# Kernel optimization log

Hardware: AMD Instinct MI355X
Metric: run time of the kernel (lower is better)

Reference implementation:

```python
import jax, jax.numpy as jnp
import numpy as np

B, N, H, W, C = 512, 16, 84, 84, 3
CNN_OUT, ATTN, GH, HEADS, POS, A_DIM = 256, 64, 128, 2, 3, 3
IN_GAT = CNN_OUT + POS  # 259
FLAT = 64 * 16 * 16     # conv output flat dim for 84x84 input


def setup_inputs() -> dict:
    key = jax.random.key(0)
    ks = jax.random.split(key, 16)
    s = 0.05
    return dict(
        cam=jax.random.uniform(ks[0], (B, H, W, C), jnp.float32),
        pos=jax.random.normal(ks[1], (B, POS), jnp.float32),
        team_pos=jax.random.normal(ks[2], (B, N, POS), jnp.float32) * 10.0,
        agent_idx=jax.random.randint(ks[3], (B,), 0, N),
        W1=jax.random.normal(ks[4], (32, C, 8, 8), jnp.float32) * s, b1=jnp.zeros((32,), jnp.float32),
        W2=jax.random.normal(ks[5], (64, 32, 4, 4), jnp.float32) * s, b2=jnp.zeros((64,), jnp.float32),
        W3=jax.random.normal(ks[6], (64, 64, 3, 3), jnp.float32) * s, b3=jnp.zeros((64,), jnp.float32),
        Wp=jax.random.normal(ks[7], (FLAT, CNN_OUT), jnp.float32) * 0.01, bp=jnp.zeros((CNN_OUT,), jnp.float32),
        Wid=jax.random.normal(ks[8], (1, ATTN), jnp.float32) * s, bid=jnp.zeros((ATTN,), jnp.float32),
        Wg=jax.random.normal(ks[9], (IN_GAT, HEADS * GH), jnp.float32) * s,
        a_src=jax.random.normal(ks[10], (HEADS, GH), jnp.float32) * s,
        a_dst=jax.random.normal(ks[11], (HEADS, GH), jnp.float32) * s,
        Wh1=jax.random.normal(ks[12], (HEADS * GH + ATTN, 256), jnp.float32) * s, bh1=jnp.zeros((256,), jnp.float32),
        Wh2=jax.random.normal(ks[13], (256, 2 * A_DIM), jnp.float32) * s, bh2=jnp.zeros((2 * A_DIM,), jnp.float32),
    )


def _conv(x, w, b, stride):
    y = jax.lax.conv_general_dilated(x, w, (stride, stride), 'VALID',
                                     dimension_numbers=('NCHW', 'OIHW', 'NCHW'))
    return jax.nn.relu(y + b[None, :, None, None])


def reference(cam, pos, team_pos, agent_idx, W1, b1, W2, b2, W3, b3, Wp, bp,
              Wid, bid, Wg, a_src, a_dst, Wh1, bh1, Wh2, bh2):
    # CNN encoder (NHWC -> NCHW)
    x = jnp.transpose(cam, (0, 3, 1, 2))
    x = _conv(x, W1, b1, 2)   # [B,32,39,39]
    x = _conv(x, W2, b2, 2)   # [B,64,18,18]
    x = _conv(x, W3, b3, 1)   # [B,64,16,16]
    cam_feat = jax.nn.relu(x.reshape(x.shape[0], -1) @ Wp + bp)  # [B,256]

    # per-node features: broadcast ego cam feat + relative team positions
    rel_pos = team_pos - pos[:, None, :]                                     # [B,N,3]
    node_feats = jnp.concatenate(
        [jnp.broadcast_to(cam_feat[:, None, :], (B, N, CNN_OUT)), rel_pos], axis=-1)  # [B,N,259]

    # adjacency: within 100m, no self-loops, self-loop added for isolated nodes
    dist = jnp.linalg.norm(team_pos[:, :, None, :] - team_pos[:, None, :, :], axis=-1)  # [B,N,N]
    eye = jnp.eye(N, dtype=node_feats.dtype)
    adj = (dist < 100.0).astype(node_feats.dtype) * (1.0 - eye)
    need_self = (adj.sum(axis=2) == 0).astype(adj.dtype)                     # [B,N]
    adj = adj + eye[None] * need_self[..., None]

    # dense multi-head GAT layer
    hN = (node_feats @ Wg).reshape(B, N, HEADS, GH)                          # [B,N,H,D]
    src = jnp.einsum('bnhd,hd->bnh', hN, a_src)
    dst = jnp.einsum('bnhd,hd->bnh', hN, a_dst)
    e = jax.nn.leaky_relu(src[:, :, None, :] + dst[:, None, :, :], 0.2)      # [B,i,j,H]
    e = jnp.where(adj[..., None] > 0, e, -1e9)
    alpha = jax.nn.softmax(e, axis=2)
    h = jnp.einsum('bijh,bjhd->bihd', alpha, hN).reshape(B, N, HEADS * GH)   # [B,N,256]
    h = jax.nn.elu(h)
    h = jnp.nan_to_num(h, nan=0.0, posinf=0.0, neginf=0.0)

    # agent-id embedding, fuse, gather own node, policy head
    id_emb = jax.nn.relu(agent_idx.astype(jnp.float32)[:, None] @ Wid + bid)  # [B,64]
    fused = jnp.concatenate([h, jnp.broadcast_to(id_emb[:, None, :], (B, N, ATTN))], axis=-1)  # [B,N,320]
    agent_feat = fused[jnp.arange(B), agent_idx]                             # [B,320]
    z = jax.nn.relu(agent_feat @ Wh1 + bh1)
    logits = z @ Wh2 + bh2                                                    # [B,6]
    return logits
```

## Files before the change

kernel.cpp:

```cpp
#include <hip/hip_runtime.h>


typedef __attribute__((ext_vector_type(8))) short bf16x8;
typedef __attribute__((ext_vector_type(4))) float f32x4;

union U4 { uint4 v; unsigned int u[4]; bf16x8 h; };

__device__ __forceinline__ unsigned short f2bf(float x) {
    unsigned int u = __float_as_uint(x);
    return (unsigned short)((u + 0x7FFFu + ((u >> 16) & 1u)) >> 16);
}
__device__ __forceinline__ unsigned int pack2(float lo, float hi) {
    return (unsigned int)f2bf(lo) | ((unsigned int)f2bf(hi) << 16);
}
__device__ __forceinline__ bf16x8 loadA(const unsigned int* __restrict__ W, int k8, int M, int oc) {
    U4 r; r.v = *(const uint4*)(W + (((size_t)k8 * M + oc) << 2));
    return r.h;
}
__device__ __forceinline__ bf16x8 loadB4(const unsigned int* __restrict__ base, size_t idx) {
    U4 r; r.v = *(const uint4*)(base + (idx << 2));
    return r.h;
}
#define MFMA(a, b, c) __builtin_amdgcn_mfma_f32_16x16x32_bf16((a), (b), (c), 0, 0, 0)

__device__ __forceinline__ int xcd_swz(int L, int nwg) {
    int q = nwg >> 3, r = nwg & 7;
    int x = L & 7, i = L >> 3;
    return (x < r ? x * (q + 1) : r * (q + 1) + (x - r) * q) + i;
}

__device__ __forceinline__ void storeK(unsigned int* __restrict__ out,
                                       size_t row, size_t BC, size_t bcol,
                                       int lg, unsigned int u0, unsigned int u1) {
    uint2 v; v.x = u0; v.y = u1;
    *(uint2*)(out + ((row * BC + bcol) << 2) + ((lg & 1) << 1)) = v;
}

__global__ __launch_bounds__(256) void prepack(
    const float* __restrict__ W1, const float* __restrict__ W2,
    const float* __restrict__ W3, const float* __restrict__ Wp,
    const float* __restrict__ Wg, const float* __restrict__ Wh1,
    unsigned int* __restrict__ W1t, unsigned int* __restrict__ W2t,
    unsigned int* __restrict__ W3t, unsigned int* __restrict__ Wpt,
    unsigned int* __restrict__ Wgt, unsigned int* __restrict__ Wh1t)
{
    int i = blockIdx.x * 256 + threadIdx.x;
    if (i < 4096) {
        int j2 = i & 3, oc = (i >> 2) & 31, k8 = i >> 7;
        int kh = k8 >> 2, kwp = k8 & 3;
        float w[2];
        #pragma unroll
        for (int e = 0; e < 2; e++) {
            int jj = 2 * j2 + e;
            int kwlo = jj >> 2, c = jj & 3;
            w[e] = (c == 3) ? 0.f
                 : W1[((oc * 3 + c) * 8 + kh) * 8 + 2 * kwp + kwlo];
        }
        W1t[i] = pack2(w[0], w[1]);
    } else if (i < 20480) {
        int j = i - 4096;
        int j2 = j & 3, oc = (j >> 2) & 63, k8 = j >> 8;
        int tap = k8 >> 2, ic = (k8 & 3) * 8 + 2 * j2;
        int kh = tap >> 2, kw = tap & 3;
        float a = W2[((oc * 32 + ic) * 4 + kh) * 4 + kw];
        float b = W2[((oc * 32 + ic + 1) * 4 + kh) * 4 + kw];
        W2t[j] = pack2(a, b);
    } else if (i < 38912) {
        int j = i - 20480;
        int j2 = j & 3, oc = (j >> 2) & 63, k8 = j >> 8;
        int tap = k8 >> 3, ic = (k8 & 7) * 8 + 2 * j2;
        int kh = tap / 3, kw = tap % 3;
        float a = W3[((oc * 64 + ic) * 3 + kh) * 3 + kw];
        float b = W3[((oc * 64 + ic + 1) * 3 + kh) * 3 + kw];
        W3t[j] = pack2(a, b);
    } else if (i < 2136064) {
        int j = i - 38912;
        int j2 = j & 3, n = (j >> 2) & 255, k8 = j >> 10;
        int s3 = k8 >> 3, oc = (k8 & 7) * 8 + 2 * j2;
        float a = Wp[(size_t)(oc * 256 + s3) * 256 + n];
        float b = Wp[(size_t)((oc + 1) * 256 + s3) * 256 + n];
        Wpt[j] = pack2(a, b);
    } else if (i < 2168832) {
        int j = i - 2136064;
        int j2 = j & 3, m = (j >> 2) & 255, k8 = j >> 10;
        int k = k8 * 8 + 2 * j2;
        Wgt[j] = pack2(Wg[k * 256 + m], Wg[(k + 1) * 256 + m]);
    } else if (i < 2209792) {
        int j = i - 2168832;
        int j2 = j & 3, m = (j >> 2) & 255, k8 = j >> 10;
        int k = k8 * 8 + 2 * j2;
        Wh1t[j] = pack2(Wh1[k * 256 + m], Wh1[(k + 1) * 256 + m]);
    }
}

__global__ __launch_bounds__(256) void transpose_cam(
    const float* __restrict__ cam, unsigned int* __restrict__ camq, int b0, int BC)
{
    __shared__ float lds[32][253];
    int yy = blockIdx.x;
    int bb = blockIdx.y * 32;
    int t = threadIdx.x;
    for (int f = t; f < 8064; f += 256) {
        int b = f / 252, p = f - b * 252;
        lds[b][p] = cam[(size_t)(b0 + bb + b) * 21168 + yy * 252 + p];
    }
    __syncthreads();
    for (int g = t; g < 1344; g += 256) {
        int b = g & 31, xp = g >> 5;
        const float* l = &lds[b][6 * xp];
        uint4 u;
        u.x = pack2(l[0], l[1]);
        u.y = pack2(l[2], 0.f);
        u.z = pack2(l[3], l[4]);
        u.w = pack2(l[5], 0.f);
        *(uint4*)(camq + (((size_t)(yy * 42 + xp) * BC + bb + b) << 2)) = u;
    }
}

__global__ __launch_bounds__(256, 3) void conv1_pair(
    const unsigned int* __restrict__ in32, const unsigned int* __restrict__ Wt,
    const float* __restrict__ bias, unsigned int* __restrict__ out32,
    int BC, int nspat)
{
    int wgid = xcd_swz(blockIdx.x, gridDim.x);
    int s = wgid % nspat;
    int bq = wgid / nspat;
    int ohp = s / 39, ow = s - ohp * 39;
    int oh0 = 2 * ohp;
    const bool has2 = (oh0 + 1) < 39;
    int wv = threadIdx.x >> 6, l = threadIdx.x & 63;
    int lg = l >> 4, lc = l & 15;
    const size_t sBC = (size_t)BC;
    size_t base = (size_t)bq * 256 + wv * 64 + lc;
    f32x4 acc0[2][4] = {}, acc1[2][4] = {};
    bf16x8 Ar0[2], Ar1[2];
    #pragma unroll
    for (int t = 0; t < 10; t++) {
        const int par = t & 1;
        bf16x8 B[4];
        if (t < 8 || has2) {
            size_t row = (size_t)((2 * oh0 + t) * 42 + ow + lg);
            #pragma unroll
            for (int g = 0; g < 4; g++)
                B[g] = loadB4(in32, row * sBC + base + g * 16);
        }
        if (t >= 2 && has2) {
            #pragma unroll
            for (int g = 0; g < 4; g++) {
                acc1[0][g] = MFMA(Ar0[par], B[g], acc1[0][g]);
                acc1[1][g] = MFMA(Ar1[par], B[g], acc1[1][g]);
            }
        }
        if (t < 8) {
            bf16x8 An0 = loadA(Wt, t * 4 + lg, 32, lc);
            bf16x8 An1 = loadA(Wt, t * 4 + lg, 32, 16 + lc);
            #pragma unroll
            for (int g = 0; g < 4; g++) {
                acc0[0][g] = MFMA(An0, B[g], acc0[0][g]);
                acc0[1][g] = MFMA(An1, B[g], acc0[1][g]);
            }
            Ar0[par] = An0; Ar1[par] = An1;
        }
    }
    int s0 = oh0 * 39 + ow;
    #pragma unroll
    for (int m = 0; m < 2; m++) {
        float4 bv = *(const float4*)(bias + m * 16 + lg * 4);
        size_t row = (size_t)s0 * 4 + 2 * m + (lg >> 1);
        #pragma unroll
        for (int g = 0; g < 4; g++) {
            f32x4 a = acc0[m][g];
            unsigned int u0 = pack2(fmaxf(a.x + bv.x, 0.f), fmaxf(a.y + bv.y, 0.f));
            unsigned int u1 = pack2(fmaxf(a.z + bv.z, 0.f), fmaxf(a.w + bv.w, 0.f));
            storeK(out32, row, sBC, base + g * 16, lg, u0, u1);
        }
        if (has2) {
            size_t row1 = row + 4 * 39;
            #pragma unroll
            for (int g = 0; g < 4; g++) {
                f32x4 a = acc1[m][g];
                unsigned int u0 = pack2(fmaxf(a.x + bv.x, 0.f), fmaxf(a.y + bv.y, 0.f));
                unsigned int u1 = pack2(fmaxf(a.z + bv.z, 0.f), fmaxf(a.w + bv.w, 0.f));
                storeK(out32, row1, sBC, base + g * 16, lg, u0, u1);
            }
        }
    }
}

__global__ __launch_bounds__(256, 3) void conv2_mfma(
    const unsigned int* __restrict__ in32, const unsigned int* __restrict__ Wt,
    const float* __restrict__ bias, unsigned int* __restrict__ out32,
    int BC, int nspat)
{
    int wgid = xcd_swz(blockIdx.x, gridDim.x);
    int s = wgid % nspat;
    int bq = wgid / nspat;
    int oh = s / 18, ow = s - oh * 18;
    int wv = threadIdx.x >> 6, l = threadIdx.x & 63;
    int lg = l >> 4, lc = l & 15;
    const size_t sBC = (size_t)BC;
    size_t base = (size_t)bq * 256 + wv * 64 + lc;
    f32x4 acc[4][4] = {};
    int ybase = 2 * oh, xbase = 2 * ow;
    #pragma unroll 1
    for (int sp = 0; sp < 8; sp++) {
        const int s0 = 2 * sp, s1 = s0 + 1;
        bf16x8 A0[4], A1[4], B0[4], B1[4];
        #pragma unroll
        for (int m = 0; m < 4; m++) {
            A0[m] = loadA(Wt, s0 * 4 + lg, 64, m * 16 + lc);
            A1[m] = loadA(Wt, s1 * 4 + lg, 64, m * 16 + lc);
        }
        {
            const int kh = s0 >> 2, kw = s0 & 3;
            size_t row = (size_t)(((ybase + kh) * 39 + xbase + kw) * 4 + lg);
            #pragma unroll
            for (int g = 0; g < 4; g++)
                B0[g] = loadB4(in32, row * sBC + base + g * 16);
        }
        {
            const int kh = s1 >> 2, kw = s1 & 3;
            size_t row = (size_t)(((ybase + kh) * 39 + xbase + kw) * 4 + lg);
            #pragma unroll
            for (int g = 0; g < 4; g++)
                B1[g] = loadB4(in32, row * sBC + base + g * 16);
        }
        #pragma unroll
        for (int m = 0; m < 4; m++)
            #pragma unroll
            for (int g = 0; g < 4; g++)
                acc[m][g] = MFMA(A0[m], B0[g], acc[m][g]);
        #pragma unroll
        for (int m = 0; m < 4; m++)
            #pragma unroll
            for (int g = 0; g < 4; g++)
                acc[m][g] = MFMA(A1[m], B1[g], acc[m][g]);
    }
    #pragma unroll
    for (int m = 0; m < 4; m++) {
        float4 bv = *(const float4*)(bias + m * 16 + lg * 4);
        size_t row = (size_t)s * 8 + 2 * m + (lg >> 1);
        #pragma unroll
        for (int g = 0; g < 4; g++) {
            f32x4 a = acc[m][g];
            unsigned int u0 = pack2(fmaxf(a.x + bv.x, 0.f), fmaxf(a.y + bv.y, 0.f));
            unsigned int u1 = pack2(fmaxf(a.z + bv.z, 0.f), fmaxf(a.w + bv.w, 0.f));
            storeK(out32, row, sBC, base + g * 16, lg, u0, u1);
        }
    }
}

__global__ __launch_bounds__(256, 3) void conv3_mfma(
    const unsigned int* __restrict__ in32, const unsigned int* __restrict__ Wt,
    const float* __restrict__ bias, unsigned int* __restrict__ out32,
    int BC, int nspat)
{
    int wgid = xcd_swz(blockIdx.x, gridDim.x);
    int s = wgid % nspat;
    int bq = wgid / nspat;
    int oh = s >> 4, ow = s & 15;
    int wv = threadIdx.x >> 6, l = threadIdx.x & 63;
    int lg = l >> 4, lc = l & 15;
    const size_t sBC = (size_t)BC;
    size_t base = (size_t)bq * 256 + wv * 64 + lc;
    f32x4 acc[4][4] = {};
    #pragma unroll 1
    for (int sp = 0; sp < 9; sp++) {
        const int s0 = 2 * sp, s1 = s0 + 1;
        const int kh = sp / 3, kw = sp - kh * 3;
        bf16x8 A0[4], A1[4], B0[4], B1[4];
        #pragma unroll
        for (int m = 0; m < 4; m++) {
            A0[m] = loadA(Wt, s0 * 4 + lg, 64, m * 16 + lc);
            A1[m] = loadA(Wt, s1 * 4 + lg, 64, m * 16 + lc);
        }
        size_t row0 = (size_t)(((oh + kh) * 18 + ow + kw) * 8 + lg);
        #pragma unroll
        for (int g = 0; g < 4; g++) {
            B0[g] = loadB4(in32, row0 * sBC + base + g * 16);
            B1[g] = loadB4(in32, (row0 + 4) * sBC + base + g * 16);
        }
        #pragma unroll
        for (int m = 0; m < 4; m++)
            #pragma unroll
            for (int g = 0; g < 4; g++)
                acc[m][g] = MFMA(A0[m], B0[g], acc[m][g]);
        #pragma unroll
        for (int m = 0; m < 4; m++)
            #pragma unroll
            for (int g = 0; g < 4; g++)
                acc[m][g] = MFMA(A1[m], B1[g], acc[m][g]);
    }
    #pragma unroll
    for (int m = 0; m < 4; m++) {
        float4 bv = *(const float4*)(bias + m * 16 + lg * 4);
        size_t row = (size_t)s * 8 + 2 * m + (lg >> 1);
        #pragma unroll
        for (int g = 0; g < 4; g++) {
            f32x4 a = acc[m][g];
            unsigned int u0 = pack2(fmaxf(a.x + bv.x, 0.f), fmaxf(a.y + bv.y, 0.f));
            unsigned int u1 = pack2(fmaxf(a.z + bv.z, 0.f), fmaxf(a.w + bv.w, 0.f));
            storeK(out32, row, sBC, base + g * 16, lg, u0, u1);
        }
    }
}

__global__ __launch_bounds__(256, 3) void proj_mfma(
    const unsigned int* __restrict__ x3, const unsigned int* __restrict__ Wpt,
    float* __restrict__ partial, int BC)
{
    int wgid = xcd_swz(blockIdx.x, gridDim.x);
    int rem = wgid & 127;
    int b128 = wgid >> 7;
    int mq = rem & 3;
    int kseg = rem >> 2;
    int wv = threadIdx.x >> 6, l = threadIdx.x & 63;
    int lg = l >> 4, lc = l & 15;
    const size_t sBC = (size_t)BC;
    size_t base = (size_t)b128 * 128 + wv * 32 + lc;
    f32x4 acc[4][2] = {};
    #pragma unroll 1
    for (int sp = 0; sp < 8; sp++) {
        const int k8b = kseg * 64 + sp * 8;
        bf16x8 A0[4], A1[4], B0[2], B1[2];
        #pragma unroll
        for (int m = 0; m < 4; m++) {
            A0[m] = loadA(Wpt, k8b + lg, 256, mq * 64 + m * 16 + lc);
            A1[m] = loadA(Wpt, k8b + 4 + lg, 256, mq * 64 + m * 16 + lc);
        }
        #pragma unroll
        for (int g = 0; g < 2; g++) {
            B0[g] = loadB4(x3, (size_t)(k8b + lg) * sBC + base + g * 16);
            B1[g] = loadB4(x3, (size_t)(k8b + 4 + lg) * sBC + base + g * 16);
        }
        #pragma unroll
        for (int m = 0; m < 4; m++)
            #pragma unroll
            for (int g = 0; g < 2; g++)
                acc[m][g] = MFMA(A0[m], B0[g], acc[m][g]);
        #pragma unroll
        for (int m = 0; m < 4; m++)
            #pragma unroll
            for (int g = 0; g < 2; g++)
                acc[m][g] = MFMA(A1[m], B1[g], acc[m][g]);
    }
    #pragma unroll
    for (int m = 0; m < 4; m++) {
        size_t row4 = (size_t)kseg * 64 + mq * 16 + m * 4 + lg;
        #pragma unroll
        for (int g = 0; g < 2; g++)
            *(f32x4*)(partial + ((row4 * sBC + base + g * 16) << 2)) = acc[m][g];
    }
}

__global__ __launch_bounds__(256) void reduce_k(
    const float* __restrict__ partial, const float* __restrict__ bp,
    unsigned int* __restrict__ cf16, int b0, int BC, int bcShift)
{
    int i = blockIdx.x * 256 + threadIdx.x;
    int bl = i & (BC - 1);
    int k8 = i >> bcShift;
    f32x4 S0 = {}, S1 = {};
    for (int seg = 0; seg < 32; seg++) {
        const float* p = partial + (((size_t)(seg * 64 + k8 * 2) * BC + bl) << 2);
        S0 += *(const f32x4*)p;
        S1 += *(const f32x4*)(p + (BC << 2));
    }
    int n = k8 * 8;
    uint4 u;
    u.x = pack2(fmaxf(S0.x + bp[n + 0], 0.f), fmaxf(S0.y + bp[n + 1], 0.f));
    u.y = pack2(fmaxf(S0.z + bp[n + 2], 0.f), fmaxf(S0.w + bp[n + 3], 0.f));
    u.z = pack2(fmaxf(S1.x + bp[n + 4], 0.f), fmaxf(S1.y + bp[n + 5], 0.f));
    u.w = pack2(fmaxf(S1.z + bp[n + 6], 0.f), fmaxf(S1.w + bp[n + 7], 0.f));
    *(uint4*)(cf16 + (((size_t)k8 * 512 + b0 + bl) << 2)) = u;
}

__global__ __launch_bounds__(64) void gat_prep(
    const unsigned int* __restrict__ cf16, const unsigned int* __restrict__ Wgt,
    float* __restrict__ hNb)
{
    int mq = blockIdx.x, bq = blockIdx.y;
    int l = threadIdx.x, lg = l >> 4, lc = l & 15;
    size_t bcol = (size_t)bq * 32 + lc;
    f32x4 acc[4][2] = {};
    #pragma unroll
    for (int sp = 0; sp < 4; sp++) {
        const int s0 = 2 * sp, s1 = s0 + 1;
        bf16x8 A0[4], A1[4], B0[2], B1[2];
        #pragma unroll
        for (int m = 0; m < 4; m++) {
            A0[m] = loadA(Wgt, s0 * 4 + lg, 256, mq * 64 + m * 16 + lc);
            A1[m] = loadA(Wgt, s1 * 4 + lg, 256, mq * 64 + m * 16 + lc);
        }
        #pragma unroll
        for (int g = 0; g < 2; g++) {
            B0[g] = loadB4(cf16, (size_t)(s0 * 4 + lg) * 512 + bcol + g * 16);
            B1[g] = loadB4(cf16, (size_t)(s1 * 4 + lg) * 512 + bcol + g * 16);
        }
        #pragma unroll
        for (int m = 0; m < 4; m++) {
            acc[m][0] = MFMA(A0[m], B0[0], acc[m][0]);
            acc[m][1] = MFMA(A0[m], B0[1], acc[m][1]);
            acc[m][0] = MFMA(A1[m], B1[0], acc[m][0]);
            acc[m][1] = MFMA(A1[m], B1[1], acc[m][1]);
        }
    }
    #pragma unroll
    for (int m = 0; m < 4; m++) {
        #pragma unroll
        for (int g = 0; g < 2; g++) {
            size_t b = (size_t)bq * 32 + g * 16 + lc;
            int row0 = mq * 64 + m * 16 + lg * 4;
            *(f32x4*)(hNb + b * 256 + row0) = acc[m][g];
        }
    }
}

__global__ __launch_bounds__(256) void gat_mid(
    const float* __restrict__ hNb, const float* __restrict__ pos,
    const float* __restrict__ tpos, const int* __restrict__ aidx,
    const float* __restrict__ Wg, const float* __restrict__ asrc, const float* __restrict__ adst,
    const float* __restrict__ Wid, const float* __restrict__ bid,
    unsigned int* __restrict__ af16)
{
    int b = blockIdx.x, t = threadIdx.x;
    __shared__ float hN[16][256];
    __shared__ float srcv[16][2], dstv[16][2];
    __shared__ float alpha[16][2];
    __shared__ float af[320];
    __shared__ unsigned int adjm_s;

    int ai = aidx[b];
    float basev = hNb[(size_t)b * 256 + t];
    float rw0 = Wg[65536 + t], rw1 = Wg[65792 + t], rw2 = Wg[66048 + t];
    float px = pos[b * 3 + 0], py = pos[b * 3 + 1], pz = pos[b * 3 + 2];
    for (int n = 0; n < 16; n++) {
        float r0 = tpos[(b * 16 + n) * 3 + 0] - px;
        float r1 = tpos[(b * 16 + n) * 3 + 1] - py;
        float r2 = tpos[(b * 16 + n) * 3 + 2] - pz;
        hN[n][t] = basev + r0 * rw0 + r1 * rw1 + r2 * rw2;
    }

    if (t < 64) {
        bool on = false;
        if (t < 16 && t != ai) {
            float dx = tpos[(b * 16 + ai) * 3 + 0] - tpos[(b * 16 + t) * 3 + 0];
            float dy = tpos[(b * 16 + ai) * 3 + 1] - tpos[(b * 16 + t) * 3 + 1];
            float dz = tpos[(b * 16 + ai) * 3 + 2] - tpos[(b * 16 + t) * 3 + 2];
            on = (dx * dx + dy * dy + dz * dz) < 10000.0f;
        }
        unsigned long long m = __ballot(on);
        if (t == 0) adjm_s = (m == 0ull) ? (1u << ai) : (unsigned int)m;
    }
    __syncthreads();

    {
        int p = t >> 3, sub = t & 7;
        int j = p >> 1, h = p & 1;
        float s1 = 0.f, s2 = 0.f;
        #pragma unroll
        for (int dd = 0; dd < 16; dd++) {
            int d = h * 128 + sub * 16 + dd;
            float v = hN[j][d];
            s1 += v * asrc[d];
            s2 += v * adst[d];
        }
        s1 += __shfl_xor(s1, 1); s1 += __shfl_xor(s1, 2); s1 += __shfl_xor(s1, 4);
        s2 += __shfl_xor(s2, 1); s2 += __shfl_xor(s2, 2); s2 += __shfl_xor(s2, 4);
        if (sub == 0) { srcv[j][h] = s1; dstv[j][h] = s2; }
    }
    __syncthreads();

    if (t < 32) {
        int j = t & 15, h = t >> 4;
        unsigned int am = adjm_s;
        float e = srcv[ai][h] + dstv[j][h];
        e = (e > 0.f) ? e : 0.2f * e;
        e = ((am >> j) & 1u) ? e : -1e9f;
        float mx = e;
        mx = fmaxf(mx, __shfl_xor(mx, 1));
        mx = fmaxf(mx, __shfl_xor(mx, 2));
        mx = fmaxf(mx, __shfl_xor(mx, 4));
        mx = fmaxf(mx, __shfl_xor(mx, 8));
        float ex = __expf(e - mx);
        float sm = ex;
        sm += __shfl_xor(sm, 1); sm += __shfl_xor(sm, 2);
        sm += __shfl_xor(sm, 4); sm += __shfl_xor(sm, 8);
        alpha[j][h] = ex / sm;
    }
    __syncthreads();

    {
        int h = t >> 7;
        float o = 0.f;
        #pragma unroll
        for (int j = 0; j < 16; j++) o += alpha[j][h] * hN[j][t];
        o = (o > 0.f) ? o : (__expf(o) - 1.f);
        af[t] = o;
    }
    if (t < 64) {
        float v = (float)ai * Wid[t] + bid[t];
        af[256 + t] = fmaxf(v, 0.f);
    }
    __syncthreads();

    if (t < 40) {
        uint4 u;
        u.x = pack2(af[t * 8 + 0], af[t * 8 + 1]);
        u.y = pack2(af[t * 8 + 2], af[t * 8 + 3]);
        u.z = pack2(af[t * 8 + 4], af[t * 8 + 5]);
        u.w = pack2(af[t * 8 + 6], af[t * 8 + 7]);
        *(uint4*)(af16 + (((size_t)t * 512 + b) << 2)) = u;
    }
}

__global__ __launch_bounds__(64) void head_mfma(
    const unsigned int* __restrict__ af16, const unsigned int* __restrict__ Wh1t,
    const float* __restrict__ bh1, float* __restrict__ zf)
{
    int mq = blockIdx.x, bq = blockIdx.y;
    int l = threadIdx.x, lg = l >> 4, lc = l & 15;
    size_t bcol = (size_t)bq * 32 + lc;
    f32x4 acc[4][2] = {};
    #pragma unroll
    for (int sp = 0; sp < 5; sp++) {
        const int s0 = 2 * sp, s1 = s0 + 1;
        bf16x8 A0[4], A1[4], B0[2], B1[2];
        #pragma unroll
        for (int m = 0; m < 4; m++) {
            A0[m] = loadA(Wh1t, s0 * 4 + lg, 256, mq * 64 + m * 16 + lc);
            A1[m] = loadA(Wh1t, s1 * 4 + lg, 256, mq * 64 + m * 16 + lc);
        }
        #pragma unroll
        for (int g = 0; g < 2; g++) {
            B0[g] = loadB4(af16, (size_t)(s0 * 4 + lg) * 512 + bcol + g * 16);
            B1[g] = loadB4(af16, (size_t)(s1 * 4 + lg) * 512 + bcol + g * 16);
        }
        #pragma unroll
        for (int m = 0; m < 4; m++) {
            acc[m][0] = MFMA(A0[m], B0[0], acc[m][0]);
            acc[m][1] = MFMA(A0[m], B0[1], acc[m][1]);
            acc[m][0] = MFMA(A1[m], B1[0], acc[m][0]);
            acc[m][1] = MFMA(A1[m], B1[1], acc[m][1]);
        }
    }
    #pragma unroll
    for (int m = 0; m < 4; m++) {
        int row0 = mq * 64 + m * 16 + lg * 4;
        float4 bv = *(const float4*)(bh1 + row0);
        #pragma unroll
        for (int g = 0; g < 2; g++) {
            f32x4 a = acc[m][g];
            size_t b = (size_t)bq * 32 + g * 16 + lc;
            float* pp = zf + (size_t)row0 * 512 + b;
            pp[0]       = fmaxf(a.x + bv.x, 0.f);
            pp[512]     = fmaxf(a.y + bv.y, 0.f);
            pp[2 * 512] = fmaxf(a.z + bv.z, 0.f);
            pp[3 * 512] = fmaxf(a.w + bv.w, 0.f);
        }
    }
}

__global__ __launch_bounds__(256) void logits_k(
    const float* __restrict__ zf, const float* __restrict__ Wh2,
    const float* __restrict__ bh2, float* __restrict__ out)
{
    __shared__ float Ws[1536];
    int t = threadIdx.x;
    int b = blockIdx.x * 256 + t;
    for (int f = t; f < 1536; f += 256) Ws[f] = Wh2[f];
    __syncthreads();
    float acc[6];
    #pragma unroll
    for (int j = 0; j < 6; j++) acc[j] = bh2[j];
    for (int k = 0; k < 256; k++) {
        float zv = zf[(size_t)k * 512 + b];
        #pragma unroll
        for (int j = 0; j < 6; j++) acc[j] += zv * Ws[k * 6 + j];
    }
    #pragma unroll
    for (int j = 0; j < 6; j++) out[b * 6 + j] = acc[j];
}

extern "C" void kernel_launch(void* const* d_in, const int* in_sizes, int n_in,
                              void* d_out, int out_size, void* d_ws, size_t ws_size,
                              hipStream_t stream)
{
    const float* cam  = (const float*)d_in[0];
    const float* pos  = (const float*)d_in[1];
    const float* tpos = (const float*)d_in[2];
    const int*   aidx = (const int*)d_in[3];
    const float* W1   = (const float*)d_in[4];
    const float* b1   = (const float*)d_in[5];
    const float* W2   = (const float*)d_in[6];
    const float* b2   = (const float*)d_in[7];
    const float* W3   = (const float*)d_in[8];
    const float* b3   = (const float*)d_in[9];
    const float* Wp   = (const float*)d_in[10];
    const float* bp   = (const float*)d_in[11];
    const float* Wid  = (const float*)d_in[12];
    const float* bid  = (const float*)d_in[13];
    const float* Wg   = (const float*)d_in[14];
    const float* asrc = (const float*)d_in[15];
    const float* adst = (const float*)d_in[16];
    const float* Wh1  = (const float*)d_in[17];
    const float* bh1  = (const float*)d_in[18];
    const float* Wh2  = (const float*)d_in[19];
    const float* bh2  = (const float*)d_in[20];
    float* out = (float*)d_out;

    int BC = 256;
    if (((size_t)54832 * 512 + 2619392) * 4 <= ws_size) BC = 512;
    int bcShift = (BC == 512) ? 9 : 8;
    int nbq2 = BC >> 8;

    unsigned int* ws32 = (unsigned int*)d_ws;
    unsigned int* RA  = ws32;
    unsigned int* RB  = RA + (size_t)14112 * BC;
    unsigned int* RC  = RB + (size_t)24336 * BC;
    float*        RD  = (float*)(RC + (size_t)8192 * BC);
    unsigned int* W1t = (unsigned int*)(RD + (size_t)8192 * BC);
    unsigned int* W2t  = W1t + 4096;
    unsigned int* W3t  = W2t + 16384;
    unsigned int* Wpt  = W3t + 18432;
    unsigned int* Wgt  = Wpt + 2097152;
    unsigned int* Wh1t = Wgt + 32768;
    unsigned int* cf16 = Wh1t + 40960;
    float*        hNb  = (float*)(cf16 + 65536);
    unsigned int* af16 = (unsigned int*)(hNb + 131072);
    float*        zf   = (float*)(af16 + 81920);

    prepack<<<8632, 256, 0, stream>>>(W1, W2, W3, Wp, Wg, Wh1,
                                      W1t, W2t, W3t, Wpt, Wgt, Wh1t);

    for (int b0 = 0; b0 < 512; b0 += BC) {
        transpose_cam<<<dim3(84, BC / 32), 256, 0, stream>>>(cam, RA, b0, BC);
        conv1_pair<<<780 * nbq2, 256, 0, stream>>>(RA, W1t, b1, RB, BC, 780);
        conv2_mfma<<<324 * nbq2, 256, 0, stream>>>(RB, W2t, b2, RA, BC, 324);
        conv3_mfma<<<256 * nbq2, 256, 0, stream>>>(RA, W3t, b3, RC, BC, 256);
        proj_mfma<<<128 * (BC >> 7), 256, 0, stream>>>(RC, Wpt, RD, BC);
        reduce_k<<<(32 * BC) / 256, 256, 0, stream>>>(RD, bp, cf16, b0, BC, bcShift);
    }
    gat_prep<<<dim3(4, 16), 64, 0, stream>>>(cf16, Wgt, hNb);
    gat_mid<<<512, 256, 0, stream>>>(hNb, pos, tpos, aidx, Wg, asrc, adst,
                                     Wid, bid, af16);
    head_mfma<<<dim3(4, 16), 64, 0, stream>>>(af16, Wh1t, bh1, zf);
    logits_k<<<2, 256, 0, stream>>>(zf, Wh2, bh2, out);
}
```

Measured before the change: 148.3 us.

## Halve conv/proj workgroup size, shrink split-K, and fuse head with logits

conv2 and conv3 now run 128-thread workgroups covering 128 batch columns each, which doubles the grid. The projection GEMM also uses 128-thread workgroups over 64 columns, but each one handles twice the K range, so there are 16 K segments instead of 32. This halves the partial-sum buffer and the reduction work. The head MFMA and logits kernels are fused into one kernel that keeps z in shared memory, removing a launch and a global round trip. The trade-off is more workgroups and less weight reuse per group in the convs, plus fewer parallel K segments in proj.

```diff
diff --git a/kernel.cpp b/kernel.cpp
--- a/kernel.cpp
+++ b/kernel.cpp
@@ -187,7 +187,7 @@
     }
 }
 
-__global__ __launch_bounds__(256, 3) void conv2_mfma(
+__global__ __launch_bounds__(128, 3) void conv2_mfma(
     const unsigned int* __restrict__ in32, const unsigned int* __restrict__ Wt,
     const float* __restrict__ bias, unsigned int* __restrict__ out32,
     int BC, int nspat)
@@ -199,7 +199,7 @@
     int wv = threadIdx.x >> 6, l = threadIdx.x & 63;
     int lg = l >> 4, lc = l & 15;
     const size_t sBC = (size_t)BC;
-    size_t base = (size_t)bq * 256 + wv * 64 + lc;
+    size_t base = (size_t)bq * 128 + wv * 64 + lc;
     f32x4 acc[4][4] = {};
     int ybase = 2 * oh, xbase = 2 * ow;
     #pragma unroll 1
@@ -250,7 +250,7 @@
     }
 }
 
-__global__ __launch_bounds__(256, 3) void conv3_mfma(
+__global__ __launch_bounds__(128, 3) void conv3_mfma(
     const unsigned int* __restrict__ in32, const unsigned int* __restrict__ Wt,
     const float* __restrict__ bias, unsigned int* __restrict__ out32,
     int BC, int nspat)
@@ -262,7 +262,7 @@
     int wv = threadIdx.x >> 6, l = threadIdx.x & 63;
     int lg = l >> 4, lc = l & 15;
     const size_t sBC = (size_t)BC;
-    size_t base = (size_t)bq * 256 + wv * 64 + lc;
+    size_t base = (size_t)bq * 128 + wv * 64 + lc;
     f32x4 acc[4][4] = {};
     #pragma unroll 1
     for (int sp = 0; sp < 9; sp++) {
@@ -305,23 +305,23 @@
     }
 }
 
-__global__ __launch_bounds__(256, 3) void proj_mfma(
+__global__ __launch_bounds__(128, 3) void proj_mfma(
     const unsigned int* __restrict__ x3, const unsigned int* __restrict__ Wpt,
     float* __restrict__ partial, int BC)
 {
     int wgid = xcd_swz(blockIdx.x, gridDim.x);
-    int rem = wgid & 127;
-    int b128 = wgid >> 7;
+    int rem = wgid & 63;
+    int b64 = wgid >> 6;
     int mq = rem & 3;
     int kseg = rem >> 2;
     int wv = threadIdx.x >> 6, l = threadIdx.x & 63;
     int lg = l >> 4, lc = l & 15;
     const size_t sBC = (size_t)BC;
-    size_t base = (size_t)b128 * 128 + wv * 32 + lc;
+    size_t base = (size_t)b64 * 64 + wv * 32 + lc;
     f32x4 acc[4][2] = {};
     #pragma unroll 1
-    for (int sp = 0; sp < 8; sp++) {
-        const int k8b = kseg * 64 + sp * 8;
+    for (int sp = 0; sp < 16; sp++) {
+        const int k8b = kseg * 128 + sp * 8;
         bf16x8 A0[4], A1[4], B0[2], B1[2];
         #pragma unroll
         for (int m = 0; m < 4; m++) {
@@ -361,7 +361,7 @@
     int bl = i & (BC - 1);
     int k8 = i >> bcShift;
     f32x4 S0 = {}, S1 = {};
-    for (int seg = 0; seg < 32; seg++) {
+    for (int seg = 0; seg < 16; seg++) {
         const float* p = partial + (((size_t)(seg * 64 + k8 * 2) * BC + bl) << 2);
         S0 += *(const f32x4*)p;
         S1 += *(const f32x4*)(p + (BC << 2));
@@ -514,12 +514,18 @@
     }
 }
 
-__global__ __launch_bounds__(64) void head_mfma(
+__global__ __launch_bounds__(256) void head_logits(
     const unsigned int* __restrict__ af16, const unsigned int* __restrict__ Wh1t,
-    const float* __restrict__ bh1, float* __restrict__ zf)
-{
-    int mq = blockIdx.x, bq = blockIdx.y;
-    int l = threadIdx.x, lg = l >> 4, lc = l & 15;
+    const float* __restrict__ bh1, const float* __restrict__ Wh2,
+    const float* __restrict__ bh2, float* __restrict__ out)
+{
+    __shared__ float zfs[256][32];
+    __shared__ float Ws[1536];
+    int bq = blockIdx.x;
+    int t = threadIdx.x;
+    int mq = t >> 6, l = t & 63, lg = l >> 4, lc = l & 15;
+    for (int f = t; f < 1536; f += 256) Ws[f] = Wh2[f];
+
     size_t bcol = (size_t)bq * 32 + lc;
     f32x4 acc[4][2] = {};
     #pragma unroll
@@ -551,35 +557,22 @@
         #pragma unroll
         for (int g = 0; g < 2; g++) {
             f32x4 a = acc[m][g];
-            size_t b = (size_t)bq * 32 + g * 16 + lc;
-            float* pp = zf + (size_t)row0 * 512 + b;
-            pp[0]       = fmaxf(a.x + bv.x, 0.f);
-            pp[512]     = fmaxf(a.y + bv.y, 0.f);
-            pp[2 * 512] = fmaxf(a.z + bv.z, 0.f);
-            pp[3 * 512] = fmaxf(a.w + bv.w, 0.f);
-        }
-    }
-}
-
-__global__ __launch_bounds__(256) void logits_k(
-    const float* __restrict__ zf, const float* __restrict__ Wh2,
-    const float* __restrict__ bh2, float* __restrict__ out)
-{
-    __shared__ float Ws[1536];
-    int t = threadIdx.x;
-    int b = blockIdx.x * 256 + t;
-    for (int f = t; f < 1536; f += 256) Ws[f] = Wh2[f];
+            int bl = g * 16 + lc;
+            zfs[row0 + 0][bl] = fmaxf(a.x + bv.x, 0.f);
+            zfs[row0 + 1][bl] = fmaxf(a.y + bv.y, 0.f);
+            zfs[row0 + 2][bl] = fmaxf(a.z + bv.z, 0.f);
+            zfs[row0 + 3][bl] = fmaxf(a.w + bv.w, 0.f);
+        }
+    }
     __syncthreads();
-    float acc[6];
-    #pragma unroll
-    for (int j = 0; j < 6; j++) acc[j] = bh2[j];
-    for (int k = 0; k < 256; k++) {
-        float zv = zf[(size_t)k * 512 + b];
-        #pragma unroll
-        for (int j = 0; j < 6; j++) acc[j] += zv * Ws[k * 6 + j];
-    }
-    #pragma unroll
-    for (int j = 0; j < 6; j++) out[b * 6 + j] = acc[j];
+
+    if (t < 192) {
+        int b = t & 31, j = t >> 5;
+        float s = bh2[j];
+        #pragma unroll 8
+        for (int k = 0; k < 256; k++) s += zfs[k][b] * Ws[k * 6 + j];
+        out[(bq * 32 + b) * 6 + j] = s;
+    }
 }
 
 extern "C" void kernel_launch(void* const* d_in, const int* in_sizes, int n_in,
@@ -610,16 +603,18 @@
     float* out = (float*)d_out;
 
     int BC = 256;
-    if (((size_t)54832 * 512 + 2619392) * 4 <= ws_size) BC = 512;
+    if (((size_t)50736 * 512 + 2488320) * 4 <= ws_size) BC = 512;
     int bcShift = (BC == 512) ? 9 : 8;
     int nbq2 = BC >> 8;
+    int nbq7 = BC >> 7;
+    int nbq6 = BC >> 6;
 
     unsigned int* ws32 = (unsigned int*)d_ws;
     unsigned int* RA  = ws32;
     unsigned int* RB  = RA + (size_t)14112 * BC;
     unsigned int* RC  = RB + (size_t)24336 * BC;
     float*        RD  = (float*)(RC + (size_t)8192 * BC);
-    unsigned int* W1t = (unsigned int*)(RD + (size_t)8192 * BC);
+    unsigned int* W1t = (unsigned int*)(RD + (size_t)4096 * BC);
     unsigned int* W2t  = W1t + 4096;
     unsigned int* W3t  = W2t + 16384;
     unsigned int* Wpt  = W3t + 18432;
@@ -628,7 +623,6 @@
     unsigned int* cf16 = Wh1t + 40960;
     float*        hNb  = (float*)(cf16 + 65536);
     unsigned int* af16 = (unsigned int*)(hNb + 131072);
-    float*        zf   = (float*)(af16 + 81920);
 
     prepack<<<8632, 256, 0, stream>>>(W1, W2, W3, Wp, Wg, Wh1,
                                       W1t, W2t, W3t, Wpt, Wgt, Wh1t);
@@ -636,14 +630,13 @@
     for (int b0 = 0; b0 < 512; b0 += BC) {
         transpose_cam<<<dim3(84, BC / 32), 256, 0, stream>>>(cam, RA, b0, BC);
         conv1_pair<<<780 * nbq2, 256, 0, stream>>>(RA, W1t, b1, RB, BC, 780);
-        conv2_mfma<<<324 * nbq2, 256, 0, stream>>>(RB, W2t, b2, RA, BC, 324);
-        conv3_mfma<<<256 * nbq2, 256, 0, stream>>>(RA, W3t, b3, RC, BC, 256);
-        proj_mfma<<<128 * (BC >> 7), 256, 0, stream>>>(RC, Wpt, RD, BC);
+        conv2_mfma<<<324 * nbq7, 128, 0, stream>>>(RB, W2t, b2, RA, BC, 324);
+        conv3_mfma<<<256 * nbq7, 128, 0, stream>>>(RA, W3t, b3, RC, BC, 256);
+        proj_mfma<<<64 * nbq6, 128, 0, stream>>>(RC, Wpt, RD, BC);
         reduce_k<<<(32 * BC) / 256, 256, 0, stream>>>(RD, bp, cf16, b0, BC, bcShift);
     }
     gat_prep<<<dim3(4, 16), 64, 0, stream>>>(cf16, Wgt, hNb);
     gat_mid<<<512, 256, 0, stream>>>(hNb, pos, tpos, aidx, Wg, asrc, adst,
                                      Wid, bid, af16);
-    head_mfma<<<dim3(4, 16), 64, 0, stream>>>(af16, Wh1t, bh1, zf);
-    logits_k<<<2, 256, 0, stream>>>(zf, Wh2, bh2, out);
-}
+    head_logits<<<16, 256, 0, stream>>>(af16, Wh1t, bh1, Wh2, bh2, out);
+}
```

After: 146.7 us (median of 2 runs). No clear change (-1.1%).
